# Kernel optimization log

Hardware: AMD Instinct MI355X
Metric: run time of the kernel (lower is better)

## Reference

```python
import jax, jax.numpy as jnp
import numpy as np

B, H, W, C = 32, 512, 512, 3


def setup_inputs() -> dict:
    key = jax.random.key(0)
    k1, k2, k3 = jax.random.split(key, 3)
    images = jax.random.normal(k1, (B, H, W, C), dtype=jnp.float32)
    # focal lengths in pixels, positive and well-conditioned
    focal = 400.0 + 200.0 * jax.random.uniform(k2, (B, 2), dtype=jnp.float32)
    # quaternion ~ identity rotation + small noise (stddev=0.01), q0 mean 1
    q = jnp.array([1.0, 0.0, 0.0, 0.0], jnp.float32) + 0.01 * jax.random.normal(k3, (4,), dtype=jnp.float32)
    return {"images": images, "focal": focal, "q": q}


def _quaternion_to_R(q):
    # matches tf_quaternion_to_R: normalize so sum(q^2)=2, then outer product
    q = q * jnp.sqrt(2.0 / jnp.sum(q * q))
    Q = q[:, None] * q[None, :]  # [4,4], Q[i,j] = q_i q_j
    return jnp.array([
        [1.0 - Q[2, 2] - Q[3, 3], Q[1, 2] - Q[3, 0], Q[1, 3] + Q[2, 0]],
        [Q[1, 2] + Q[3, 0], 1.0 - Q[1, 1] - Q[3, 3], Q[2, 3] - Q[1, 0]],
        [Q[1, 3] - Q[2, 0], Q[2, 3] + Q[1, 0], 1.0 - Q[1, 1] - Q[2, 2]],
    ])


def _forward(images, focal, q):
    R = _quaternion_to_R(q)  # [3,3]
    d = jnp.concatenate([focal, jnp.ones((focal.shape[0], 1), focal.dtype)], axis=1)  # [B,3]
    # H = K @ R @ inv(K) with K = diag(d):  H[b,i,j] = d[b,i] * R[i,j] / d[b,j]
    Hm = R[None, :, :] * d[:, :, None] / d[:, None, :]  # [B,3,3]

    origin_x = jnp.float32(W / 2)
    origin_y = jnp.float32(H / 2)
    xs = jnp.arange(W, dtype=jnp.float32) - origin_x  # [W]
    ys = jnp.arange(H, dtype=jnp.float32) - origin_y  # [H]
    x, y = jnp.meshgrid(xs, ys)  # [H,W] each
    ps = jnp.stack([x.ravel(), y.ravel(), jnp.ones(H * W, jnp.float32)], axis=0)  # [3,N]

    ps_w = jnp.einsum('bij,jn->bin', Hm, ps)  # [B,3,N]
    x_w = (ps_w[:, 0, :] / ps_w[:, 2, :]).reshape(-1, H, W) + origin_x  # [B,H,W]
    y_w = (ps_w[:, 1, :] / ps_w[:, 2, :]).reshape(-1, H, W) + origin_y  # [B,H,W]

    # bilinear resampler (tf.contrib.resampler): zero outside image bounds
    x0 = jnp.floor(x_w)
    y0 = jnp.floor(y_w)
    wx = x_w - x0
    wy = y_w - y0
    x0i = x0.astype(jnp.int32)
    y0i = y0.astype(jnp.int32)

    b = jnp.arange(images.shape[0])[:, None, None]

    def corner(yi, xi, w):
        valid = (xi >= 0) & (xi <= W - 1) & (yi >= 0) & (yi <= H - 1)
        g = images[b, jnp.clip(yi, 0, H - 1), jnp.clip(xi, 0, W - 1)]  # [B,H,W,C]
        return g * (w * valid.astype(images.dtype))[..., None]

    out = (corner(y0i, x0i, (1.0 - wx) * (1.0 - wy))
           + corner(y0i, x0i + 1, wx * (1.0 - wy))
           + corner(y0i + 1, x0i, (1.0 - wx) * wy)
           + corner(y0i + 1, x0i + 1, wx * wy))
    return out


def reference(images, focal, q):
    return _forward(images, focal, q)
```

## Files before the change

kernel.cpp:

```cpp
#include <hip/hip_runtime.h>
#include <hip/hip_bf16.h>


#define IMG_H 512
#define IMG_W 512
#define IMG_C 3
#define NB    32

__global__ __launch_bounds__(256) void warp_kernel(
    const float* __restrict__ images,
    const float* __restrict__ focal,
    const float* __restrict__ q,
    float* __restrict__ out)
{
    const unsigned bid  = blockIdx.x;
    const unsigned xcd  = bid & 7u;
    const unsigned slot = bid >> 3;
    const unsigned virt = xcd * 4096u + slot;
    const int b        = (int)(virt >> 10);
    const unsigned rem = virt & 1023u;
    const int y        = (int)(rem >> 1);
    const int xbase    = (int)(rem & 1u) * 256;

    const int tid = threadIdx.x;

    __shared__ float sH[9];
    __shared__ float s_out[256 * 3];

    if (tid == 0) {
        float q0 = q[0], q1 = q[1], q2 = q[2], q3 = q[3];
        float s = sqrtf(2.0f / (q0*q0 + q1*q1 + q2*q2 + q3*q3));
        q0 *= s; q1 *= s; q2 *= s; q3 *= s;
        float R00 = 1.0f - q2*q2 - q3*q3;
        float R01 = q1*q2 - q3*q0;
        float R02 = q1*q3 + q2*q0;
        float R10 = q1*q2 + q3*q0;
        float R11 = 1.0f - q1*q1 - q3*q3;
        float R12 = q2*q3 - q1*q0;
        float R20 = q1*q3 - q2*q0;
        float R21 = q2*q3 + q1*q0;
        float R22 = 1.0f - q1*q1 - q2*q2;
        float d0 = focal[b*2 + 0];
        float d1 = focal[b*2 + 1];
        float d2 = 1.0f;
        sH[0] = (R00*d0)/d0; sH[1] = (R01*d0)/d1; sH[2] = (R02*d0)/d2;
        sH[3] = (R10*d1)/d0; sH[4] = (R11*d1)/d1; sH[5] = (R12*d1)/d2;
        sH[6] = (R20*d2)/d0; sH[7] = (R21*d2)/d1; sH[8] = (R22*d2)/d2;
    }
    __syncthreads();

    const float xs = (float)(xbase + tid) - 256.0f;
    const float ys = (float)y - 256.0f;

    const float h0 = sH[0], h1 = sH[1], h2 = sH[2];
    const float h3 = sH[3], h4 = sH[4], h5 = sH[5];
    const float h6 = sH[6], h7 = sH[7], h8 = sH[8];

    float p0 = h0*xs + h1*ys + h2;
    float p1 = h3*xs + h4*ys + h5;
    float p2 = h6*xs + h7*ys + h8;

    float xw = p0 / p2 + 256.0f;
    float yw = p1 / p2 + 256.0f;

    float x0f = floorf(xw);
    float y0f = floorf(yw);
    float wx = xw - x0f;
    float wy = yw - y0f;
    int x0 = (int)x0f;
    int y0 = (int)y0f;

    float w00 = (1.0f - wx) * (1.0f - wy);
    float w01 = wx * (1.0f - wy);
    float w10 = (1.0f - wx) * wy;
    float w11 = wx * wy;

    const float* img_b = images + (size_t)b * (IMG_H * IMG_W * IMG_C);

    float acc0 = 0.0f, acc1 = 0.0f, acc2 = 0.0f;

    #define CORNER(yi, xi, w) do {                                         \
        int _yi = (yi), _xi = (xi);                                        \
        bool _valid = (_xi >= 0) & (_xi <= IMG_W-1) &                      \
                      (_yi >= 0) & (_yi <= IMG_H-1);                       \
        int _yc = min(max(_yi, 0), IMG_H-1);                               \
        int _xc = min(max(_xi, 0), IMG_W-1);                               \
        const float* _p = img_b + ((size_t)_yc * IMG_W + _xc) * IMG_C;     \
        float _wv = _valid ? (w) : 0.0f;                                   \
        acc0 += _p[0] * _wv;                                               \
        acc1 += _p[1] * _wv;                                               \
        acc2 += _p[2] * _wv;                                               \
    } while (0)

    CORNER(y0,     x0,     w00);
    CORNER(y0,     x0 + 1, w01);
    CORNER(y0 + 1, x0,     w10);
    CORNER(y0 + 1, x0 + 1, w11);

    #undef CORNER

    s_out[tid*3 + 0] = acc0;
    s_out[tid*3 + 1] = acc1;
    s_out[tid*3 + 2] = acc2;
    __syncthreads();

    if (tid < 192) {
        float4 v = *reinterpret_cast<const float4*>(&s_out[tid * 4]);
        float4* outp = reinterpret_cast<float4*>(
            out + (((size_t)b * IMG_H + y) * IMG_W + xbase) * IMG_C);
        outp[tid] = v;
    }
}

extern "C" void kernel_launch(void* const* d_in, const int* in_sizes, int n_in,
                              void* d_out, int out_size, void* d_ws, size_t ws_size,
                              hipStream_t stream) {
    const float* images = (const float*)d_in[0];
    const float* focal  = (const float*)d_in[1];
    const float* q      = (const float*)d_in[2];
    float* out = (float*)d_out;

    dim3 grid(32768);
    dim3 block(256);
    warp_kernel<<<grid, block, 0, stream>>>(images, focal, q, out);
}
```

Measured before the change: 37.94 us.

## Process full image row per block with two pixels per thread and nontemporal stores

Each block now handles a whole 512-pixel row, with every thread computing two output pixels, so the grid shrinks by half. This amortizes the per-block homography setup and syncs and increases memory-level parallelism per thread by issuing all twelve corner loads up front. Output is written with nontemporal vector stores, and address math uses 32-bit unsigned arithmetic. The trade-offs are higher register pressure and doubled shared memory per block, which may reduce occupancy.

```diff
diff --git a/kernel.cpp b/kernel.cpp
--- a/kernel.cpp
+++ b/kernel.cpp
@@ -6,6 +6,8 @@
 #define IMG_W 512
 #define IMG_C 3
 #define NB    32
+
+typedef float f32x4 __attribute__((ext_vector_type(4)));
 
 __global__ __launch_bounds__(256) void warp_kernel(
     const float* __restrict__ images,
@@ -16,16 +18,14 @@
     const unsigned bid  = blockIdx.x;
     const unsigned xcd  = bid & 7u;
     const unsigned slot = bid >> 3;
-    const unsigned virt = xcd * 4096u + slot;
-    const int b        = (int)(virt >> 10);
-    const unsigned rem = virt & 1023u;
-    const int y        = (int)(rem >> 1);
-    const int xbase    = (int)(rem & 1u) * 256;
+    const unsigned virt = xcd * 2048u + slot;
+    const int b = (int)(virt >> 9);
+    const int y = (int)(virt & 511u);
 
     const int tid = threadIdx.x;
 
     __shared__ float sH[9];
-    __shared__ float s_out[256 * 3];
+    __shared__ float s_out[IMG_W * IMG_C];
 
     if (tid == 0) {
         float q0 = q[0], q1 = q[1], q2 = q[2], q3 = q[3];
@@ -42,73 +42,75 @@
         float R22 = 1.0f - q1*q1 - q2*q2;
         float d0 = focal[b*2 + 0];
         float d1 = focal[b*2 + 1];
-        float d2 = 1.0f;
-        sH[0] = (R00*d0)/d0; sH[1] = (R01*d0)/d1; sH[2] = (R02*d0)/d2;
-        sH[3] = (R10*d1)/d0; sH[4] = (R11*d1)/d1; sH[5] = (R12*d1)/d2;
-        sH[6] = (R20*d2)/d0; sH[7] = (R21*d2)/d1; sH[8] = (R22*d2)/d2;
+        sH[0] = (R00*d0)/d0; sH[1] = (R01*d0)/d1; sH[2] = (R02*d0);
+        sH[3] = (R10*d1)/d0; sH[4] = (R11*d1)/d1; sH[5] = (R12*d1);
+        sH[6] = R20/d0;      sH[7] = R21/d1;      sH[8] = R22;
     }
     __syncthreads();
-
-    const float xs = (float)(xbase + tid) - 256.0f;
-    const float ys = (float)y - 256.0f;
 
     const float h0 = sH[0], h1 = sH[1], h2 = sH[2];
     const float h3 = sH[3], h4 = sH[4], h5 = sH[5];
     const float h6 = sH[6], h7 = sH[7], h8 = sH[8];
 
-    float p0 = h0*xs + h1*ys + h2;
-    float p1 = h3*xs + h4*ys + h5;
-    float p2 = h6*xs + h7*ys + h8;
+    const float ys = (float)y - 256.0f;
+    const float* __restrict__ img_b = images + (unsigned)b * (IMG_H * IMG_W * IMG_C);
 
-    float xw = p0 / p2 + 256.0f;
-    float yw = p1 / p2 + 256.0f;
-
-    float x0f = floorf(xw);
-    float y0f = floorf(yw);
-    float wx = xw - x0f;
-    float wy = yw - y0f;
-    int x0 = (int)x0f;
-    int y0 = (int)y0f;
-
-    float w00 = (1.0f - wx) * (1.0f - wy);
-    float w01 = wx * (1.0f - wy);
-    float w10 = (1.0f - wx) * wy;
-    float w11 = wx * wy;
-
-    const float* img_b = images + (size_t)b * (IMG_H * IMG_W * IMG_C);
-
-    float acc0 = 0.0f, acc1 = 0.0f, acc2 = 0.0f;
-
-    #define CORNER(yi, xi, w) do {                                         \
-        int _yi = (yi), _xi = (xi);                                        \
-        bool _valid = (_xi >= 0) & (_xi <= IMG_W-1) &                      \
-                      (_yi >= 0) & (_yi <= IMG_H-1);                       \
-        int _yc = min(max(_yi, 0), IMG_H-1);                               \
-        int _xc = min(max(_xi, 0), IMG_W-1);                               \
-        const float* _p = img_b + ((size_t)_yc * IMG_W + _xc) * IMG_C;     \
-        float _wv = _valid ? (w) : 0.0f;                                   \
-        acc0 += _p[0] * _wv;                                               \
-        acc1 += _p[1] * _wv;                                               \
-        acc2 += _p[2] * _wv;                                               \
+    #define SAMPLE(PX, A0, A1, A2) do {                                        \
+        const float xs = (float)(PX) - 256.0f;                                 \
+        float p0 = h0*xs + h1*ys + h2;                                         \
+        float p1 = h3*xs + h4*ys + h5;                                         \
+        float p2 = h6*xs + h7*ys + h8;                                         \
+        float xw = p0 / p2 + 256.0f;                                           \
+        float yw = p1 / p2 + 256.0f;                                           \
+        float x0f = floorf(xw), y0f = floorf(yw);                              \
+        float wx = xw - x0f,   wy = yw - y0f;                                  \
+        int x0 = (int)x0f, y0i = (int)y0f;                                     \
+        int x1 = x0 + 1,  y1i = y0i + 1;                                       \
+        bool vx0 = (x0 >= 0) & (x0 <= IMG_W-1);                                \
+        bool vx1 = (x1 >= 0) & (x1 <= IMG_W-1);                                \
+        bool vy0 = (y0i >= 0) & (y0i <= IMG_H-1);                              \
+        bool vy1 = (y1i >= 0) & (y1i <= IMG_H-1);                              \
+        unsigned xc0 = (unsigned)min(max(x0, 0), IMG_W-1);                     \
+        unsigned xc1 = (unsigned)min(max(x1, 0), IMG_W-1);                     \
+        unsigned yc0 = (unsigned)min(max(y0i, 0), IMG_H-1);                    \
+        unsigned yc1 = (unsigned)min(max(y1i, 0), IMG_H-1);                    \
+        const float* p00 = img_b + (yc0 * IMG_W + xc0) * IMG_C;                \
+        const float* p01 = img_b + (yc0 * IMG_W + xc1) * IMG_C;                \
+        const float* p10 = img_b + (yc1 * IMG_W + xc0) * IMG_C;                \
+        const float* p11 = img_b + (yc1 * IMG_W + xc1) * IMG_C;                \
+        float a00 = p00[0], a01 = p00[1], a02 = p00[2];                        \
+        float b00 = p01[0], b01 = p01[1], b02 = p01[2];                        \
+        float c00 = p10[0], c01 = p10[1], c02 = p10[2];                        \
+        float d00 = p11[0], d01 = p11[1], d02 = p11[2];                        \
+        float w00 = (vx0 & vy0) ? (1.0f - wx) * (1.0f - wy) : 0.0f;            \
+        float w01 = (vx1 & vy0) ? wx * (1.0f - wy)          : 0.0f;            \
+        float w10 = (vx0 & vy1) ? (1.0f - wx) * wy          : 0.0f;            \
+        float w11 = (vx1 & vy1) ? wx * wy                   : 0.0f;            \
+        A0 = a00*w00 + b00*w01 + c00*w10 + d00*w11;                            \
+        A1 = a01*w00 + b01*w01 + c01*w10 + d01*w11;                            \
+        A2 = a02*w00 + b02*w01 + c02*w10 + d02*w11;                            \
     } while (0)
 
-    CORNER(y0,     x0,     w00);
-    CORNER(y0,     x0 + 1, w01);
-    CORNER(y0 + 1, x0,     w10);
-    CORNER(y0 + 1, x0 + 1, w11);
+    float o0a, o1a, o2a, o0b, o1b, o2b;
+    SAMPLE(tid,        o0a, o1a, o2a);
+    SAMPLE(tid + 256,  o0b, o1b, o2b);
+    #undef SAMPLE
 
-    #undef CORNER
-
-    s_out[tid*3 + 0] = acc0;
-    s_out[tid*3 + 1] = acc1;
-    s_out[tid*3 + 2] = acc2;
+    s_out[tid*3 + 0] = o0a;
+    s_out[tid*3 + 1] = o1a;
+    s_out[tid*3 + 2] = o2a;
+    s_out[(tid + 256)*3 + 0] = o0b;
+    s_out[(tid + 256)*3 + 1] = o1b;
+    s_out[(tid + 256)*3 + 2] = o2b;
     __syncthreads();
 
-    if (tid < 192) {
-        float4 v = *reinterpret_cast<const float4*>(&s_out[tid * 4]);
-        float4* outp = reinterpret_cast<float4*>(
-            out + (((size_t)b * IMG_H + y) * IMG_W + xbase) * IMG_C);
-        outp[tid] = v;
+    f32x4* outp = reinterpret_cast<f32x4*>(
+        out + ((unsigned)(b * IMG_H + y)) * (IMG_W * IMG_C));
+    f32x4 v0 = *reinterpret_cast<const f32x4*>(&s_out[tid * 4]);
+    __builtin_nontemporal_store(v0, &outp[tid]);
+    if (tid < 128) {
+        f32x4 v1 = *reinterpret_cast<const f32x4*>(&s_out[(256 + tid) * 4]);
+        __builtin_nontemporal_store(v1, &outp[256 + tid]);
     }
 }
 
@@ -120,7 +122,7 @@
     const float* q      = (const float*)d_in[2];
     float* out = (float*)d_out;
 
-    dim3 grid(32768);
+    dim3 grid(16384);
     dim3 block(256);
     warp_kernel<<<grid, block, 0, stream>>>(images, focal, q, out);
 }
```

Result: faster. 33.30 us (-12.2%).
